# Kernel optimization log

Hardware: AMD Instinct MI355X
Metric: run time of the kernel (lower is better)

Reference implementation:

```python
import jax, jax.numpy as jnp
import numpy as np
from jax import lax

N_PTS = 1_000_000
K_VOL = 27
C_IN = 64
C_OUT = 64


def setup_inputs() -> dict:
    key = jax.random.key(0)
    k1, k2, k3, k4 = jax.random.split(key, 4)
    features = jax.random.normal(k1, (N_PTS, C_IN), dtype=jnp.float32)
    # kernel param, uniform(-std, std) as in reset_parameters
    std = 1.0 / np.sqrt(C_IN * K_VOL)
    kernel = jax.random.uniform(k2, (K_VOL, C_IN, C_OUT), dtype=jnp.float32,
                                minval=-std, maxval=std)
    # out->in kernel map: for each output voxel and kernel offset, the index
    # of the contributing input voxel; mask marks which offsets are valid.
    kmap = jax.random.randint(k3, (N_PTS, K_VOL), 0, N_PTS, dtype=jnp.int64)
    kmap_mask = jax.random.randint(k4, (N_PTS, K_VOL), 0, 2, dtype=jnp.int32)
    return {"features": features, "kernel": kernel,
            "kmap": kmap, "kmap_mask": kmap_mask}


def reference(features, kernel, kmap, kmap_mask):
    # Sparse conv in output-stationary dataflow: for each kernel offset k,
    # gather input rows via kmap[:, k], mask invalid neighbors, apply the
    # per-offset GEMM kernel[k], and accumulate into the output rows.
    mask = kmap_mask.astype(features.dtype)  # [N, K]

    def body(acc, xs):
        idx, m, w = xs               # idx: [N], m: [N], w: [C_in, C_out]
        g = features[idx] * m[:, None]   # masked gather [N, C_in]
        return acc + g @ w, None

    acc0 = jnp.zeros((kmap.shape[0], kernel.shape[2]), dtype=features.dtype)
    out, _ = lax.scan(body, acc0, (kmap.T, mask.T, kernel))
    return out
```

## Files before the change

kernel.cpp:

```cpp
#include <hip/hip_runtime.h>
#include <hip/hip_bf16.h>

typedef short bf16x8 __attribute__((ext_vector_type(8)));
typedef float f32x4  __attribute__((ext_vector_type(4)));
typedef int   i32x4  __attribute__((ext_vector_type(4)));

#define N_PTS  1000000
#define K_VOL  27
#define C_IN   64
#define C_OUT  64
#define ROWS_PER_BLOCK 256
#define NIDX   (ROWS_PER_BLOCK * K_VOL)

static __device__ __forceinline__ short f2bf(float x) {
    __hip_bfloat16 h = __float2bfloat16(x);
    return *(short*)&h;
}

__global__ __launch_bounds__(256) void cvt_feat(const float* __restrict__ f,
                                                __hip_bfloat16* __restrict__ o,
                                                int n8) {
    int id = blockIdx.x * 256 + threadIdx.x;
    if (id >= n8) return;
    const float4* src = (const float4*)f;
    float4 a = src[id * 2 + 0];
    float4 b = src[id * 2 + 1];
    bf16x8 v;
    v[0] = f2bf(a.x); v[1] = f2bf(a.y); v[2] = f2bf(a.z); v[3] = f2bf(a.w);
    v[4] = f2bf(b.x); v[5] = f2bf(b.y); v[6] = f2bf(b.z); v[7] = f2bf(b.w);
    ((bf16x8*)o)[id] = v;
}

__global__ void repack_w(const float* __restrict__ W,
                         __hip_bfloat16* __restrict__ outw) {
    int id = blockIdx.x * 256 + threadIdx.x;
    if (id >= K_VOL * 2 * 4 * 64) return;
    int lane = id & 63;
    int t    = (id >> 6) & 3;
    int s    = (id >> 8) & 1;
    int k    = id >> 9;
    int ci0  = s * 32 + (lane >> 4) * 8;
    int co   = t * 16 + (lane & 15);
    const float* src = W + (k * C_IN + ci0) * C_OUT + co;
    bf16x8 v;
#pragma unroll
    for (int j = 0; j < 8; ++j) v[j] = f2bf(src[j * C_OUT]);
    ((bf16x8*)outw)[id] = v;
}

__global__ __launch_bounds__(256) void sconv_kernel(
    const __hip_bfloat16* __restrict__ feat,
    const int* __restrict__ kmap,
    const int* __restrict__ kmask,
    const __hip_bfloat16* __restrict__ wfrag,
    float* __restrict__ out) {

    __shared__ int s_idx[NIDX];

    const int tid = threadIdx.x;
    const int rb  = blockIdx.x * ROWS_PER_BLOCK;
    const size_t base27 = (size_t)rb * K_VOL;
    const bool full = (rb + ROWS_PER_BLOCK <= N_PTS);

    if (full) {
        const i32x4* kmap4  = (const i32x4*)(kmap  + base27);
        const i32x4* kmask4 = (const i32x4*)(kmask + base27);
        i32x4* s4 = (i32x4*)s_idx;
        for (int i = tid; i < NIDX / 4; i += 256) {
            i32x4 m = kmask4[i];
            i32x4 v = kmap4[i];
            i32x4 r;
            r[0] = m[0] ? v[0] : -1;
            r[1] = m[1] ? v[1] : -1;
            r[2] = m[2] ? v[2] : -1;
            r[3] = m[3] ? v[3] : -1;
            s4[i] = r;
        }
    } else {
        const int nvalid = (N_PTS - rb) * K_VOL;
        for (int i = tid; i < NIDX; i += 256) {
            int r = -1;
            if (i < nvalid) {
                int m = kmask[base27 + i];
                r = m ? kmap[base27 + i] : -1;
            }
            s_idx[i] = r;
        }
    }
    __syncthreads();

    const int lane = tid & 63;
    const int wave = tid >> 6;
    const int mrow = lane & 15;
    const int g    = lane >> 4;

    const bf16x8* __restrict__ f8 = (const bf16x8*)feat;
    const bf16x8* w8 = (const bf16x8*)wfrag + lane;

    f32x4 acc[4][4];
#pragma unroll
    for (int t = 0; t < 4; ++t)
#pragma unroll
        for (int c = 0; c < 4; ++c) acc[t][c] = (f32x4){0.f, 0.f, 0.f, 0.f};

    const int* sidx = s_idx + (wave * 64 + mrow) * K_VOL;

#pragma unroll 1
    for (int k = 0; k < K_VOL; ++k) {
        bf16x8 a0[4], a1[4];
#pragma unroll
        for (int t = 0; t < 4; ++t) {
            int idx = sidx[t * 16 * K_VOL + k];
            a0[t] = (bf16x8){0, 0, 0, 0, 0, 0, 0, 0};
            a1[t] = (bf16x8){0, 0, 0, 0, 0, 0, 0, 0};
            if (idx >= 0) {
                const bf16x8* fr = f8 + (size_t)idx * 8 + g;
                a0[t] = fr[0];
                a1[t] = fr[4];
            }
        }
        const bf16x8* wb = w8 + (size_t)k * 512;
        bf16x8 b00 = wb[0 * 64];
        bf16x8 b01 = wb[1 * 64];
        bf16x8 b02 = wb[2 * 64];
        bf16x8 b03 = wb[3 * 64];
        bf16x8 b10 = wb[4 * 64];
        bf16x8 b11 = wb[5 * 64];
        bf16x8 b12 = wb[6 * 64];
        bf16x8 b13 = wb[7 * 64];

#pragma unroll
        for (int t = 0; t < 4; ++t) {
            acc[t][0] = __builtin_amdgcn_mfma_f32_16x16x32_bf16(a0[t], b00, acc[t][0], 0, 0, 0);
            acc[t][1] = __builtin_amdgcn_mfma_f32_16x16x32_bf16(a0[t], b01, acc[t][1], 0, 0, 0);
            acc[t][2] = __builtin_amdgcn_mfma_f32_16x16x32_bf16(a0[t], b02, acc[t][2], 0, 0, 0);
            acc[t][3] = __builtin_amdgcn_mfma_f32_16x16x32_bf16(a0[t], b03, acc[t][3], 0, 0, 0);
            acc[t][0] = __builtin_amdgcn_mfma_f32_16x16x32_bf16(a1[t], b10, acc[t][0], 0, 0, 0);
            acc[t][1] = __builtin_amdgcn_mfma_f32_16x16x32_bf16(a1[t], b11, acc[t][1], 0, 0, 0);
            acc[t][2] = __builtin_amdgcn_mfma_f32_16x16x32_bf16(a1[t], b12, acc[t][2], 0, 0, 0);
            acc[t][3] = __builtin_amdgcn_mfma_f32_16x16x32_bf16(a1[t], b13, acc[t][3], 0, 0, 0);
        }
    }

    const int orow0 = rb + wave * 64 + g * 4;
#pragma unroll
    for (int t = 0; t < 4; ++t) {
        const int rowb = orow0 + t * 16;
#pragma unroll
        for (int j = 0; j < 4; ++j) {
            const int row = rowb + j;
            if (full || row < N_PTS) {
                size_t r = (size_t)row * C_OUT + mrow;
                out[r +  0] = acc[t][0][j];
                out[r + 16] = acc[t][1][j];
                out[r + 32] = acc[t][2][j];
                out[r + 48] = acc[t][3][j];
            }
        }
    }
}

extern "C" void kernel_launch(void* const* d_in, const int* in_sizes, int n_in,
                              void* d_out, int out_size, void* d_ws, size_t ws_size,
                              hipStream_t stream) {
    const float* feat32 = (const float*)d_in[0];
    const float* W      = (const float*)d_in[1];
    const int*   kmap   = (const int*)d_in[2];
    const int*   kmask  = (const int*)d_in[3];
    float*       out    = (float*)d_out;

    __hip_bfloat16* featbf = (__hip_bfloat16*)d_ws;
    __hip_bfloat16* wfrag  = (__hip_bfloat16*)((char*)d_ws +
                              (size_t)N_PTS * C_IN * sizeof(__hip_bfloat16));

    const int n8 = N_PTS * C_IN / 8;
    cvt_feat<<<(n8 + 255) / 256, 256, 0, stream>>>(feat32, featbf, n8);

    const int repack_threads = K_VOL * 2 * 4 * 64;
    repack_w<<<(repack_threads + 255) / 256, 256, 0, stream>>>(W, wfrag);

    const int nblocks = (N_PTS + ROWS_PER_BLOCK - 1) / ROWS_PER_BLOCK;
    sconv_kernel<<<nblocks, 256, 0, stream>>>(featbf, kmap, kmask, wfrag, out);
}
```

Baseline: 857.3 us.

## Split index staging into two phases and double-buffer weights in LDS

Index staging is split into two phases (14 and 13 offsets), which roughly halves the LDS footprint for the index table. Each wave now loads a quarter of the next offset's weight fragments into a double-buffered LDS array instead of every wave loading all weights from global memory. Launch bounds request 4 blocks per CU to raise occupancy. The cost is a __syncthreads per kernel offset, scalar non-vectorized index loads with divisions, and an extra barrier for the second staging phase.

```diff
diff --git a/kernel.cpp b/kernel.cpp
--- a/kernel.cpp
+++ b/kernel.cpp
@@ -10,7 +10,7 @@
 #define C_IN   64
 #define C_OUT  64
 #define ROWS_PER_BLOCK 256
-#define NIDX   (ROWS_PER_BLOCK * K_VOL)
+#define KS     14
 
 static __device__ __forceinline__ short f2bf(float x) {
     __hip_bfloat16 h = __float2bfloat16(x);
@@ -48,46 +48,39 @@
     ((bf16x8*)outw)[id] = v;
 }
 
-__global__ __launch_bounds__(256) void sconv_kernel(
+template<int KN>
+static __device__ __forceinline__ void stage_sidx(int* s_idx,
+                                                  const int* __restrict__ kmap,
+                                                  const int* __restrict__ kmask,
+                                                  int base27, int kb,
+                                                  int tid, int lastrow) {
+    for (int i = tid; i < ROWS_PER_BLOCK * KN; i += 256) {
+        int row = i / KN;
+        int kk  = i - row * KN;
+        int r   = -1;
+        if (row < lastrow) {
+            int gi = base27 + row * K_VOL + kb + kk;
+            int m  = kmask[gi];
+            r = m ? kmap[gi] : -1;
+        }
+        s_idx[row * KS + kk] = r;
+    }
+}
+
+__global__ __launch_bounds__(256, 4) void sconv_kernel(
     const __hip_bfloat16* __restrict__ feat,
     const int* __restrict__ kmap,
     const int* __restrict__ kmask,
     const __hip_bfloat16* __restrict__ wfrag,
     float* __restrict__ out) {
 
-    __shared__ int s_idx[NIDX];
+    __shared__ int   s_idx[ROWS_PER_BLOCK * KS];
+    __shared__ short s_b[2][8 * 512];
 
     const int tid = threadIdx.x;
     const int rb  = blockIdx.x * ROWS_PER_BLOCK;
-    const size_t base27 = (size_t)rb * K_VOL;
-    const bool full = (rb + ROWS_PER_BLOCK <= N_PTS);
-
-    if (full) {
-        const i32x4* kmap4  = (const i32x4*)(kmap  + base27);
-        const i32x4* kmask4 = (const i32x4*)(kmask + base27);
-        i32x4* s4 = (i32x4*)s_idx;
-        for (int i = tid; i < NIDX / 4; i += 256) {
-            i32x4 m = kmask4[i];
-            i32x4 v = kmap4[i];
-            i32x4 r;
-            r[0] = m[0] ? v[0] : -1;
-            r[1] = m[1] ? v[1] : -1;
-            r[2] = m[2] ? v[2] : -1;
-            r[3] = m[3] ? v[3] : -1;
-            s4[i] = r;
-        }
-    } else {
-        const int nvalid = (N_PTS - rb) * K_VOL;
-        for (int i = tid; i < NIDX; i += 256) {
-            int r = -1;
-            if (i < nvalid) {
-                int m = kmask[base27 + i];
-                r = m ? kmap[base27 + i] : -1;
-            }
-            s_idx[i] = r;
-        }
-    }
-    __syncthreads();
+    const int base27  = rb * K_VOL;
+    const int lastrow = min(ROWS_PER_BLOCK, N_PTS - rb);
 
     const int lane = tid & 63;
     const int wave = tid >> 6;
@@ -95,7 +88,19 @@
     const int g    = lane >> 4;
 
     const bf16x8* __restrict__ f8 = (const bf16x8*)feat;
-    const bf16x8* w8 = (const bf16x8*)wfrag + lane;
+    const bf16x8* __restrict__ w8 = (const bf16x8*)wfrag;
+
+    const int c0 = wave * 2 + 0;
+    const int c1 = wave * 2 + 1;
+
+    {
+        bf16x8 br0 = w8[c0 * 64 + lane];
+        bf16x8 br1 = w8[c1 * 64 + lane];
+        ((bf16x8*)s_b[0])[c0 * 64 + lane] = br0;
+        ((bf16x8*)s_b[0])[c1 * 64 + lane] = br1;
+    }
+    stage_sidx<KS>(s_idx, kmap, kmask, base27, 0, tid, lastrow);
+    __syncthreads();
 
     f32x4 acc[4][4];
 #pragma unroll
@@ -103,42 +108,75 @@
 #pragma unroll
         for (int c = 0; c < 4; ++c) acc[t][c] = (f32x4){0.f, 0.f, 0.f, 0.f};
 
-    const int* sidx = s_idx + (wave * 64 + mrow) * K_VOL;
-
+    const int* sidx = s_idx + (wave * 64 + mrow) * KS;
+
+#pragma unroll
+    for (int ph = 0; ph < 2; ++ph) {
+        const int kb = ph ? KS : 0;
+        const int kn = ph ? (K_VOL - KS) : KS;
+        if (ph) {
+            stage_sidx<K_VOL - KS>(s_idx, kmap, kmask, base27, KS, tid, lastrow);
+            __syncthreads();
+        }
 #pragma unroll 1
-    for (int k = 0; k < K_VOL; ++k) {
-        bf16x8 a0[4], a1[4];
-#pragma unroll
-        for (int t = 0; t < 4; ++t) {
-            int idx = sidx[t * 16 * K_VOL + k];
-            a0[t] = (bf16x8){0, 0, 0, 0, 0, 0, 0, 0};
-            a1[t] = (bf16x8){0, 0, 0, 0, 0, 0, 0, 0};
-            if (idx >= 0) {
-                const bf16x8* fr = f8 + (size_t)idx * 8 + g;
-                a0[t] = fr[0];
-                a1[t] = fr[4];
-            }
-        }
-        const bf16x8* wb = w8 + (size_t)k * 512;
-        bf16x8 b00 = wb[0 * 64];
-        bf16x8 b01 = wb[1 * 64];
-        bf16x8 b02 = wb[2 * 64];
-        bf16x8 b03 = wb[3 * 64];
-        bf16x8 b10 = wb[4 * 64];
-        bf16x8 b11 = wb[5 * 64];
-        bf16x8 b12 = wb[6 * 64];
-        bf16x8 b13 = wb[7 * 64];
-
-#pragma unroll
-        for (int t = 0; t < 4; ++t) {
-            acc[t][0] = __builtin_amdgcn_mfma_f32_16x16x32_bf16(a0[t], b00, acc[t][0], 0, 0, 0);
-            acc[t][1] = __builtin_amdgcn_mfma_f32_16x16x32_bf16(a0[t], b01, acc[t][1], 0, 0, 0);
-            acc[t][2] = __builtin_amdgcn_mfma_f32_16x16x32_bf16(a0[t], b02, acc[t][2], 0, 0, 0);
-            acc[t][3] = __builtin_amdgcn_mfma_f32_16x16x32_bf16(a0[t], b03, acc[t][3], 0, 0, 0);
-            acc[t][0] = __builtin_amdgcn_mfma_f32_16x16x32_bf16(a1[t], b10, acc[t][0], 0, 0, 0);
-            acc[t][1] = __builtin_amdgcn_mfma_f32_16x16x32_bf16(a1[t], b11, acc[t][1], 0, 0, 0);
-            acc[t][2] = __builtin_amdgcn_mfma_f32_16x16x32_bf16(a1[t], b12, acc[t][2], 0, 0, 0);
-            acc[t][3] = __builtin_amdgcn_mfma_f32_16x16x32_bf16(a1[t], b13, acc[t][3], 0, 0, 0);
+        for (int kk = 0; kk < kn; ++kk) {
+            const int k   = kb + kk;
+            const int cur = k & 1;
+            const bool pf = (k + 1 < K_VOL);
+
+            bf16x8 br0, br1;
+            if (pf) {
+                const bf16x8* wn = w8 + (size_t)(k + 1) * 512;
+                br0 = wn[c0 * 64 + lane];
+                br1 = wn[c1 * 64 + lane];
+            }
+
+            bf16x8 a0[4], a1[4];
+#pragma unroll
+            for (int t = 0; t < 4; ++t) {
+                int idx = sidx[t * 16 * KS + kk];
+                a0[t] = (bf16x8){0, 0, 0, 0, 0, 0, 0, 0};
+                a1[t] = (bf16x8){0, 0, 0, 0, 0, 0, 0, 0};
+                if (idx >= 0) {
+                    const bf16x8* fr = f8 + (size_t)idx * 8 + g;
+                    a0[t] = fr[0];
+                    a1[t] = fr[4];
+                }
+            }
+
+            const bf16x8* sb = (const bf16x8*)s_b[cur];
+            {
+                bf16x8 b00 = sb[0 * 64 + lane];
+                bf16x8 b01 = sb[1 * 64 + lane];
+                bf16x8 b02 = sb[2 * 64 + lane];
+                bf16x8 b03 = sb[3 * 64 + lane];
+#pragma unroll
+                for (int t = 0; t < 4; ++t) {
+                    acc[t][0] = __builtin_amdgcn_mfma_f32_16x16x32_bf16(a0[t], b00, acc[t][0], 0, 0, 0);
+                    acc[t][1] = __builtin_amdgcn_mfma_f32_16x16x32_bf16(a0[t], b01, acc[t][1], 0, 0, 0);
+                    acc[t][2] = __builtin_amdgcn_mfma_f32_16x16x32_bf16(a0[t], b02, acc[t][2], 0, 0, 0);
+                    acc[t][3] = __builtin_amdgcn_mfma_f32_16x16x32_bf16(a0[t], b03, acc[t][3], 0, 0, 0);
+                }
+            }
+            {
+                bf16x8 b10 = sb[4 * 64 + lane];
+                bf16x8 b11 = sb[5 * 64 + lane];
+                bf16x8 b12 = sb[6 * 64 + lane];
+                bf16x8 b13 = sb[7 * 64 + lane];
+#pragma unroll
+                for (int t = 0; t < 4; ++t) {
+                    acc[t][0] = __builtin_amdgcn_mfma_f32_16x16x32_bf16(a1[t], b10, acc[t][0], 0, 0, 0);
+                    acc[t][1] = __builtin_amdgcn_mfma_f32_16x16x32_bf16(a1[t], b11, acc[t][1], 0, 0, 0);
+                    acc[t][2] = __builtin_amdgcn_mfma_f32_16x16x32_bf16(a1[t], b12, acc[t][2], 0, 0, 0);
+                    acc[t][3] = __builtin_amdgcn_mfma_f32_16x16x32_bf16(a1[t], b13, acc[t][3], 0, 0, 0);
+                }
+            }
+
+            if (pf) {
+                ((bf16x8*)s_b[cur ^ 1])[c0 * 64 + lane] = br0;
+                ((bf16x8*)s_b[cur ^ 1])[c1 * 64 + lane] = br1;
+            }
+            __syncthreads();
         }
     }
 
@@ -149,7 +187,7 @@
 #pragma unroll
         for (int j = 0; j < 4; ++j) {
             const int row = rowb + j;
-            if (full || row < N_PTS) {
+            if (row < N_PTS) {
                 size_t r = (size_t)row * C_OUT + mrow;
                 out[r +  0] = acc[t][0][j];
                 out[r + 16] = acc[t][1][j];
```

Measured after the change: 1.106 ms. 1.29x slower.
